# Kernel tuning notes

Measured on AMD Instinct MI355X. Metric: run time of the kernel, lower is better.

The kernel has to match this reference:

```python
import jax, jax.numpy as jnp
import numpy as np

N, DEG, F_IN, H = 50000, 16, 128, 32
E = N * DEG


def _linear_params(key, out_f, in_f):
    kw, kb = jax.random.split(key)
    s = 1.0 / np.sqrt(in_f)
    W = jax.random.uniform(kw, (out_f, in_f), jnp.float32, -s, s)
    b = jax.random.uniform(kb, (out_f,), jnp.float32, -s, s)
    return W, b


def setup_inputs() -> dict:
    key = jax.random.key(0)
    ks = jax.random.split(key, 12)
    X = jax.random.normal(ks[0], (N, F_IN), jnp.float32)
    # DEG distinct nonzero offsets shared by all rows -> unique (src,dst) pairs,
    # so the COO tensor is already coalesced (no duplicate indices).
    offsets = jax.random.permutation(ks[1], jnp.arange(1, N))[:DEG]
    src = jnp.repeat(jnp.arange(N, dtype=jnp.int32), DEG)
    dst = ((src.reshape(N, DEG) + offsets[None, :].astype(jnp.int32)) % N).reshape(-1)
    D = jax.ops.segment_sum(jnp.ones((E,), jnp.float32), src, num_segments=N)
    wn1p, bn1p = _linear_params(ks[2], H, F_IN)      # convN1.pass_map
    wn1s, bn1s = _linear_params(ks[3], H, F_IN)      # convN1.self_map
    we1p, be1p = _linear_params(ks[4], H, 2 * H)     # convE1.pass_map
    we1s, be1s = _linear_params(ks[5], H, F_IN)      # convE1.self_map
    wn2p, bn2p = _linear_params(ks[6], H, H)         # convN2.pass_map
    wn2s, bn2s = _linear_params(ks[7], H, H)         # convN2.self_map
    we2p, be2p = _linear_params(ks[8], H, 2 * H)     # convE2.pass_map
    we2s, be2s = _linear_params(ks[9], H, H)         # convE2.self_map
    wc, bc = _linear_params(ks[10], 1, H)            # classifier
    return dict(X=X, src=src, dst=dst, D=D,
                wn1p=wn1p, bn1p=bn1p, wn1s=wn1s, bn1s=bn1s,
                we1p=we1p, be1p=be1p, we1s=we1s, be1s=be1s,
                wn2p=wn2p, bn2p=bn2p, wn2s=wn2s, bn2s=bn2s,
                we2p=we2p, be2p=be2p, we2s=we2s, be2s=be2s,
                wc=wc, bc=bc)


def reference(X, src, dst, D,
              wn1p, bn1p, wn1s, bn1s,
              we1p, be1p, we1s, be1s,
              wn2p, bn2p, wn2s, bn2s,
              we2p, be2p, we2s, be2s,
              wc, bc):
    n = X.shape[0]

    def node_conv(vals, Xn, wp, bp, ws, bs):
        # torch.sparse.sum(A, dim=1): sum edge values per source row
        Asum = jax.ops.segment_sum(vals, src, num_segments=n)
        return jax.nn.relu((Asum / D[:, None]) @ wp.T + bp + Xn @ ws.T + bs)

    def edge_conv(vals, Xn, wp, bp, ws, bs):
        X1, X2 = Xn[src], Xn[dst]
        Ef = jnp.concatenate([(X1 - X2) * 0.5, (X1 + X2) * 0.5], axis=-1)
        return jax.nn.relu(Ef @ wp.T + bp + vals @ ws.T + bs)

    # add_graph: edge features = |X[src] - X[dst]|
    vals0 = jnp.abs(X[src] - X[dst])            # (E, F_IN)
    X0 = jnp.zeros_like(X)                       # forward zeros node features
    Xn1 = node_conv(vals0, X0, wn1p, bn1p, wn1s, bn1s)   # (N, 32)
    vals1 = edge_conv(vals0, Xn1, we1p, be1p, we1s, be1s)  # (E, 32)
    Xn2 = node_conv(vals1, Xn1, wn2p, bn2p, wn2s, bn2s)  # (N, 32)
    vals2 = edge_conv(vals1, Xn2, we2p, be2p, we2s, be2s)  # (E, 32)
    SX = jax.nn.sigmoid(vals2 @ wc.T + bc)[:, 0]          # (E,)
    return SX
```

## Files before the change

kernel.cpp:

```cpp
#include <hip/hip_runtime.h>

#define DEG 16
#define F_IN 128
#define H 32
#define CH 16

typedef __attribute__((ext_vector_type(8))) _Float16 f16x8;
typedef __attribute__((ext_vector_type(4))) float f32x4;
typedef __attribute__((ext_vector_type(4))) int i32x4;

union HF4 { _Float16 h[4]; uint2 u; };
union HS  { _Float16 f; unsigned short s; };

__device__ __forceinline__ float relu_f(float x) { return fmaxf(x, 0.0f); }

__device__ __forceinline__ f16x8 habs8(f16x8 a) {
    union { f16x8 h; i32x4 i; } u; u.h = a;
#pragma unroll
    for (int k = 0; k < 4; ++k) u.i[k] &= 0x7FFF7FFF;
    return u.h;
}
__device__ __forceinline__ unsigned short f2h_s(float x) {
    HS v; v.f = (_Float16)x; return v.s;
}
__device__ __forceinline__ float h2f_s(unsigned short s) {
    HS v; v.s = s; return (float)v.f;
}

__global__ __launch_bounds__(256) void k_xhalf(
    const float* __restrict__ X, _Float16* __restrict__ Xh, long n8)
{
    const long t = (long)blockIdx.x * 256 + threadIdx.x;
    if (t >= n8) return;
    const float4* p = (const float4*)X + t * 2;
    const float4 a = p[0], b = p[1];
    f16x8 h;
    h[0] = (_Float16)a.x; h[1] = (_Float16)a.y; h[2] = (_Float16)a.z; h[3] = (_Float16)a.w;
    h[4] = (_Float16)b.x; h[5] = (_Float16)b.y; h[6] = (_Float16)b.z; h[7] = (_Float16)b.w;
    *(f16x8*)(Xh + t * 8) = h;
}

__global__ __launch_bounds__(256) void k_prep(
    const float* __restrict__ we1s, const float* __restrict__ we1p,
    const float* __restrict__ be1p, const float* __restrict__ be1s,
    const float* __restrict__ we2p, const float* __restrict__ we2s,
    const float* __restrict__ be2p, const float* __restrict__ be2s,
    const float* __restrict__ wn1p, const float* __restrict__ bn1p,
    const float* __restrict__ bn1s,
    const float* __restrict__ wn2p, const float* __restrict__ bn2p,
    const float* __restrict__ wn2s, const float* __restrict__ bn2s,
    _Float16* __restrict__ Wcat1, _Float16* __restrict__ Wcat2,
    _Float16* __restrict__ Wn1ph,
    _Float16* __restrict__ Wn2ph, _Float16* __restrict__ Wn2sh,
    float* __restrict__ bias1, float* __restrict__ bias2,
    float* __restrict__ biasn1, float* __restrict__ biasn2)
{
    const int tid = threadIdx.x;
    for (int idx = tid; idx < 32 * 192; idx += 256) {
        const int n = idx / 192, k = idx - n * 192;
        float w;
        if (k < 128)       w = we1s[n * 128 + k];
        else if (k < 160)  w = 0.5f * we1p[n * 64 + (k - 128)];
        else               w = 0.5f * we1p[n * 64 + 32 + (k - 160)];
        Wcat1[idx] = (_Float16)w;
    }
    for (int idx = tid; idx < 32 * 96; idx += 256) {
        const int n = idx / 96, k = idx - n * 96;
        float w;
        if (k < 32)       w = 0.5f * we2p[n * 64 + k];
        else if (k < 64)  w = 0.5f * we2p[n * 64 + 32 + (k - 32)];
        else              w = we2s[n * 32 + (k - 64)];
        Wcat2[idx] = (_Float16)w;
    }
    for (int idx = tid; idx < 32 * 128; idx += 256)
        Wn1ph[idx] = (_Float16)wn1p[idx];
    for (int idx = tid; idx < 32 * 32; idx += 256) {
        Wn2ph[idx] = (_Float16)wn2p[idx];
        Wn2sh[idx] = (_Float16)wn2s[idx];
    }
    if (tid < H) {
        bias1[tid]  = be1p[tid] + be1s[tid];
        bias2[tid]  = be2p[tid] + be2s[tid];
        biasn1[tid] = bn1p[tid] + bn1s[tid];
        biasn2[tid] = bn2p[tid] + bn2s[tid];
    }
}

__global__ __launch_bounds__(256) void k_p1(
    const _Float16* __restrict__ Xh, const int* __restrict__ dst,
    const float* __restrict__ D,
    const _Float16* __restrict__ Wcat1, const _Float16* __restrict__ Wn1ph,
    const float* __restrict__ biasn1,
    _Float16* __restrict__ t1h, _Float16* __restrict__ Xn1h, int N)
{
    __shared__ int dsL[16 * 17];
    __shared__ float UacS[4][16 * 33];
    const int tid = threadIdx.x;
    const int wave = tid >> 6, lane = tid & 63;
    const int i0 = blockIdx.x * CH;
    {
        const int mm = tid >> 4, j = tid & 15;
        const int nd = (i0 + mm < N) ? (i0 + mm) : (N - 1);
        dsL[mm * 17 + j] = dst[nd * DEG + j];
    }
    __syncthreads();
    const int m = lane & 15, g = lane >> 4;
    const int srow = (i0 + m < N) ? (i0 + m) : (N - 1);

    f16x8 sv[4];
#pragma unroll
    for (int kb = 0; kb < 4; ++kb)
        sv[kb] = *(const f16x8*)(Xh + (size_t)srow * F_IN + kb * 32 + g * 8);
    int dj[4];
#pragma unroll
    for (int jj = 0; jj < 4; ++jj) dj[jj] = dsL[m * 17 + wave * 4 + jj];
    f16x8 tv[4][4];
#pragma unroll
    for (int jj = 0; jj < 4; ++jj)
#pragma unroll
        for (int kb = 0; kb < 4; ++kb)
            tv[jj][kb] = *(const f16x8*)(Xh + (size_t)dj[jj] * F_IN + kb * 32 + g * 8);
    f16x8 Bs[4][2], Bn[4][2];
#pragma unroll
    for (int kb = 0; kb < 4; ++kb)
#pragma unroll
        for (int t = 0; t < 2; ++t) {
            Bs[kb][t] = *(const f16x8*)(Wcat1 + (t * 16 + m) * 192 + kb * 32 + g * 8);
            Bn[kb][t] = *(const f16x8*)(Wn1ph + (t * 16 + m) * 128 + kb * 32 + g * 8);
        }

    f32x4 cn0 = {0.f,0.f,0.f,0.f}, cn1 = {0.f,0.f,0.f,0.f};
#pragma unroll
    for (int jj = 0; jj < 4; ++jj) {
        f32x4 cs0 = {0.f,0.f,0.f,0.f}, cs1 = {0.f,0.f,0.f,0.f};
#pragma unroll
        for (int kb = 0; kb < 4; ++kb) {
            const f16x8 a = habs8(sv[kb] - tv[jj][kb]);
            cs0 = __builtin_amdgcn_mfma_f32_16x16x32_f16(a, Bs[kb][0], cs0, 0, 0, 0);
            cs1 = __builtin_amdgcn_mfma_f32_16x16x32_f16(a, Bs[kb][1], cs1, 0, 0, 0);
            cn0 = __builtin_amdgcn_mfma_f32_16x16x32_f16(a, Bn[kb][0], cn0, 0, 0, 0);
            cn1 = __builtin_amdgcn_mfma_f32_16x16x32_f16(a, Bn[kb][1], cn1, 0, 0, 0);
        }
        const size_t tb = ((size_t)blockIdx.x * 16 + wave * 4 + jj) * 512;
        HF4 a;
#pragma unroll
        for (int r = 0; r < 4; ++r) a.h[r] = (_Float16)cs0[r];
        *(uint2*)(t1h + tb + lane * 4) = a.u;
#pragma unroll
        for (int r = 0; r < 4; ++r) a.h[r] = (_Float16)cs1[r];
        *(uint2*)(t1h + tb + 256 + lane * 4) = a.u;
    }
#pragma unroll
    for (int r = 0; r < 4; ++r) {
        UacS[wave][(g * 4 + r) * 33 + m]      = cn0[r];
        UacS[wave][(g * 4 + r) * 33 + 16 + m] = cn1[r];
    }
    __syncthreads();
    {
        const int mm = tid >> 4, c = tid & 15;
        float u0 = 0.f, u1 = 0.f;
#pragma unroll
        for (int w = 0; w < 4; ++w) {
            u0 += UacS[w][mm * 33 + c];
            u1 += UacS[w][mm * 33 + 16 + c];
        }
        if (i0 + mm < N) {
            const float invD = 1.0f / D[i0 + mm];
            Xn1h[(size_t)(i0 + mm) * H + c]      = (_Float16)relu_f(u0 * invD + biasn1[c]);
            Xn1h[(size_t)(i0 + mm) * H + 16 + c] = (_Float16)relu_f(u1 * invD + biasn1[16 + c]);
        }
    }
}

__global__ __launch_bounds__(256) void k_p2(
    const int* __restrict__ dst, const _Float16* __restrict__ Xn1h,
    const _Float16* __restrict__ Wcat1, const float* __restrict__ bias1,
    const _Float16* __restrict__ Wn2ph, const _Float16* __restrict__ Wn2sh,
    const float* __restrict__ biasn2, const float* __restrict__ D,
    _Float16* t1v1,
    _Float16* __restrict__ Xn2h, int N)
{
    __shared__ int dsL[16 * 17];
    __shared__ unsigned short RP[4][16 * 40];
    __shared__ float AacS[4][16 * 33];
    __shared__ unsigned short AsumH[16 * 40];
    const int tid = threadIdx.x;
    const int wave = tid >> 6, lane = tid & 63;
    const int i0 = blockIdx.x * CH;
    {
        const int mm = tid >> 4, j = tid & 15;
        const int nd = (i0 + mm < N) ? (i0 + mm) : (N - 1);
        dsL[mm * 17 + j] = dst[nd * DEG + j];
    }
    __syncthreads();
    const int m = lane & 15, g = lane >> 4;
    const int srow = (i0 + m < N) ? (i0 + m) : (N - 1);

    const f16x8 x1 = *(const f16x8*)(Xn1h + (size_t)srow * H + g * 8);
    int dj[4];
#pragma unroll
    for (int jj = 0; jj < 4; ++jj) dj[jj] = dsL[m * 17 + wave * 4 + jj];
    f16x8 x2[4];
#pragma unroll
    for (int jj = 0; jj < 4; ++jj)
        x2[jj] = *(const f16x8*)(Xn1h + (size_t)dj[jj] * H + g * 8);
    uint2 ta[4], tbv[4];
#pragma unroll
    for (int jj = 0; jj < 4; ++jj) {
        const size_t tb = ((size_t)blockIdx.x * 16 + wave * 4 + jj) * 512;
        ta[jj]  = *(const uint2*)(t1v1 + tb + lane * 4);
        tbv[jj] = *(const uint2*)(t1v1 + tb + 256 + lane * 4);
    }
    f16x8 Bf[2][2];
#pragma unroll
    for (int kb = 0; kb < 2; ++kb)
#pragma unroll
        for (int t = 0; t < 2; ++t)
            Bf[kb][t] = *(const f16x8*)(Wcat1 + (t * 16 + m) * 192 + (4 + kb) * 32 + g * 8);

    const float b0 = bias1[m], b1v = bias1[16 + m];
    float sA0[4] = {0.f,0.f,0.f,0.f}, sA1[4] = {0.f,0.f,0.f,0.f};
    unsigned short* L = RP[wave];
#pragma unroll
    for (int jj = 0; jj < 4; ++jj) {
        f32x4 c0, c1;
        { HF4 a; a.u = ta[jj];
#pragma unroll
          for (int r = 0; r < 4; ++r) c0[r] = (float)a.h[r];
          a.u = tbv[jj];
#pragma unroll
          for (int r = 0; r < 4; ++r) c1[r] = (float)a.h[r]; }
        const f16x8 ad = x1 - x2[jj];
        const f16x8 aS = x1 + x2[jj];
        c0 = __builtin_amdgcn_mfma_f32_16x16x32_f16(ad, Bf[0][0], c0, 0, 0, 0);
        c1 = __builtin_amdgcn_mfma_f32_16x16x32_f16(ad, Bf[0][1], c1, 0, 0, 0);
        c0 = __builtin_amdgcn_mfma_f32_16x16x32_f16(aS, Bf[1][0], c0, 0, 0, 0);
        c1 = __builtin_amdgcn_mfma_f32_16x16x32_f16(aS, Bf[1][1], c1, 0, 0, 0);
#pragma unroll
        for (int r = 0; r < 4; ++r) {
            const float v0 = relu_f(c0[r] + b0);
            const float v1 = relu_f(c1[r] + b1v);
            L[(g * 4 + r) * 40 + m]      = f2h_s(v0);
            L[(g * 4 + r) * 40 + 16 + m] = f2h_s(v1);
            sA0[r] += v0; sA1[r] += v1;
        }
        const size_t tb = ((size_t)blockIdx.x * 16 + wave * 4 + jj) * 512;
        const int rr = lane >> 2, q = lane & 3;
        const i32x4 v = *(const i32x4*)(L + rr * 40 + q * 8);
        *(i32x4*)(t1v1 + tb + rr * 32 + q * 8) = v;
    }
#pragma unroll
    for (int r = 0; r < 4; ++r) {
        AacS[wave][(g * 4 + r) * 33 + m]      = sA0[r];
        AacS[wave][(g * 4 + r) * 33 + 16 + m] = sA1[r];
    }
    __syncthreads();
    {
        const int mm = tid >> 4, c = tid & 15;
        float a0 = 0.f, a1 = 0.f;
#pragma unroll
        for (int w = 0; w < 4; ++w) {
            a0 += AacS[w][mm * 33 + c];
            a1 += AacS[w][mm * 33 + 16 + c];
        }
        const int nd = (i0 + mm < N) ? (i0 + mm) : (N - 1);
        const float invD = 1.0f / D[nd];
        AsumH[mm * 40 + c]      = f2h_s(a0 * invD);
        AsumH[mm * 40 + 16 + c] = f2h_s(a1 * invD);
    }
    __syncthreads();
    if (wave == 0) {
        const f16x8 aF = *(const f16x8*)((const _Float16*)AsumH + m * 40 + g * 8);
        f16x8 Bp[2], Bs2[2];
#pragma unroll
        for (int t = 0; t < 2; ++t) {
            Bp[t]  = *(const f16x8*)(Wn2ph + (t * 16 + m) * H + g * 8);
            Bs2[t] = *(const f16x8*)(Wn2sh + (t * 16 + m) * H + g * 8);
        }
        f32x4 c0 = {0.f,0.f,0.f,0.f}, c1 = {0.f,0.f,0.f,0.f};
        c0 = __builtin_amdgcn_mfma_f32_16x16x32_f16(aF, Bp[0], c0, 0, 0, 0);
        c1 = __builtin_amdgcn_mfma_f32_16x16x32_f16(aF, Bp[1], c1, 0, 0, 0);
        c0 = __builtin_amdgcn_mfma_f32_16x16x32_f16(x1, Bs2[0], c0, 0, 0, 0);
        c1 = __builtin_amdgcn_mfma_f32_16x16x32_f16(x1, Bs2[1], c1, 0, 0, 0);
        const float bp0 = biasn2[m], bp1 = biasn2[16 + m];
#pragma unroll
        for (int r = 0; r < 4; ++r) {
            const int node = i0 + g * 4 + r;
            if (node < N) {
                Xn2h[(size_t)node * H + m]      = (_Float16)relu_f(c0[r] + bp0);
                Xn2h[(size_t)node * H + 16 + m] = (_Float16)relu_f(c1[r] + bp1);
            }
        }
    }
}

__global__ __launch_bounds__(256) void k_p3(
    const _Float16* __restrict__ Xn2h, const int* __restrict__ dst,
    const _Float16* __restrict__ vals1,
    const _Float16* __restrict__ Wcat2, const float* __restrict__ bias2,
    const float* __restrict__ wc, const float* __restrict__ bc,
    float* __restrict__ out, int N)
{
    __shared__ int dsL[16 * 17];
    __shared__ float outS[16 * 17];
    const int tid = threadIdx.x;
    const int wave = tid >> 6, lane = tid & 63;
    const int i0 = blockIdx.x * CH;
    {
        const int mm = tid >> 4, j = tid & 15;
        const int nd = (i0 + mm < N) ? (i0 + mm) : (N - 1);
        dsL[mm * 17 + j] = dst[nd * DEG + j];
    }
    __syncthreads();
    const int m = lane & 15, g = lane >> 4;
    const int srow = (i0 + m < N) ? (i0 + m) : (N - 1);

    const f16x8 x1 = *(const f16x8*)(Xn2h + (size_t)srow * H + g * 8);
    int dj[4];
#pragma unroll
    for (int jj = 0; jj < 4; ++jj) dj[jj] = dsL[m * 17 + wave * 4 + jj];
    f16x8 x2[4], av[4];
#pragma unroll
    for (int jj = 0; jj < 4; ++jj) {
        x2[jj] = *(const f16x8*)(Xn2h + (size_t)dj[jj] * H + g * 8);
        const size_t tb = ((size_t)blockIdx.x * 16 + wave * 4 + jj) * 512;
        av[jj] = *(const f16x8*)(vals1 + tb + m * 32 + g * 8);
    }
    f16x8 Bf[3][2];
#pragma unroll
    for (int kb = 0; kb < 3; ++kb)
#pragma unroll
        for (int t = 0; t < 2; ++t)
            Bf[kb][t] = *(const f16x8*)(Wcat2 + (t * 16 + m) * 96 + kb * 32 + g * 8);

    const float b0 = bias2[m], b1v = bias2[16 + m];
    const float w0 = wc[m], w1 = wc[16 + m];
#pragma unroll
    for (int jj = 0; jj < 4; ++jj) {
        const f16x8 ad = x1 - x2[jj];
        const f16x8 aS = x1 + x2[jj];
        f32x4 c0 = {0.f,0.f,0.f,0.f}, c1 = {0.f,0.f,0.f,0.f};
        c0 = __builtin_amdgcn_mfma_f32_16x16x32_f16(ad,     Bf[0][0], c0, 0, 0, 0);
        c1 = __builtin_amdgcn_mfma_f32_16x16x32_f16(ad,     Bf[0][1], c1, 0, 0, 0);
        c0 = __builtin_amdgcn_mfma_f32_16x16x32_f16(aS,     Bf[1][0], c0, 0, 0, 0);
        c1 = __builtin_amdgcn_mfma_f32_16x16x32_f16(aS,     Bf[1][1], c1, 0, 0, 0);
        c0 = __builtin_amdgcn_mfma_f32_16x16x32_f16(av[jj], Bf[2][0], c0, 0, 0, 0);
        c1 = __builtin_amdgcn_mfma_f32_16x16x32_f16(av[jj], Bf[2][1], c1, 0, 0, 0);

        float sr[4];
#pragma unroll
        for (int r = 0; r < 4; ++r)
            sr[r] = relu_f(c0[r] + b0) * w0 + relu_f(c1[r] + b1v) * w1;
#pragma unroll
        for (int mask = 1; mask < 16; mask <<= 1) {
#pragma unroll
            for (int r = 0; r < 4; ++r)
                sr[r] += __shfl_xor(sr[r], mask);
        }
        if (m == 0) {
#pragma unroll
            for (int r = 0; r < 4; ++r)
                outS[(g * 4 + r) * 17 + (wave * 4 + jj)] = sr[r];
        }
    }
    __syncthreads();
    {
        const int mm = tid >> 4;
        if (i0 + mm < N) {
            const float sx = outS[mm * 17 + (tid & 15)] + bc[0];
            out[(size_t)i0 * DEG + tid] = 1.0f / (1.0f + __expf(-sx));
        }
    }
}

extern "C" void kernel_launch(void* const* d_in, const int* in_sizes, int n_in,
                              void* d_out, int out_size, void* d_ws, size_t ws_size,
                              hipStream_t stream)
{
    const float* X    = (const float*)d_in[0];
    const int*   dst  = (const int*)  d_in[2];
    const float* D    = (const float*)d_in[3];
    const float* wn1p = (const float*)d_in[4];
    const float* bn1p = (const float*)d_in[5];
    const float* bn1s = (const float*)d_in[7];
    const float* we1p = (const float*)d_in[8];
    const float* be1p = (const float*)d_in[9];
    const float* we1s = (const float*)d_in[10];
    const float* be1s = (const float*)d_in[11];
    const float* wn2p = (const float*)d_in[12];
    const float* bn2p = (const float*)d_in[13];
    const float* wn2s = (const float*)d_in[14];
    const float* bn2s = (const float*)d_in[15];
    const float* we2p = (const float*)d_in[16];
    const float* be2p = (const float*)d_in[17];
    const float* we2s = (const float*)d_in[18];
    const float* be2s = (const float*)d_in[19];
    const float* wc   = (const float*)d_in[20];
    const float* bc   = (const float*)d_in[21];

    const int N = in_sizes[3];
    const int nbC = (N + CH - 1) / CH;
    const size_t Epad = (size_t)nbC * CH * DEG;

    char* w = (char*)d_ws;
    _Float16* t1v1  = (_Float16*)w;  w += Epad * H * 2;
    _Float16* Xh    = (_Float16*)w;  w += (size_t)N * F_IN * 2;
    _Float16* Xn1h  = (_Float16*)w;  w += (size_t)N * H * 2;
    _Float16* Xn2h  = (_Float16*)w;  w += (size_t)N * H * 2;
    _Float16* Wcat1 = (_Float16*)w;  w += 32 * 192 * 2;
    _Float16* Wcat2 = (_Float16*)w;  w += 32 * 96 * 2;
    _Float16* Wn1ph = (_Float16*)w;  w += 32 * 128 * 2;
    _Float16* Wn2ph = (_Float16*)w;  w += 32 * 32 * 2;
    _Float16* Wn2sh = (_Float16*)w;  w += 32 * 32 * 2;
    float* bias1  = (float*)w;       w += H * 4;
    float* bias2  = (float*)w;       w += H * 4;
    float* biasn1 = (float*)w;       w += H * 4;
    float* biasn2 = (float*)w;       w += H * 4;
    float* outp = (float*)d_out;

    const long n8 = (long)N * F_IN / 8;
    const int nbX = (int)((n8 + 255) / 256);

    k_xhalf<<<nbX, 256, 0, stream>>>(X, Xh, n8);
    k_prep<<<1, 256, 0, stream>>>(we1s, we1p, be1p, be1s, we2p, we2s, be2p, be2s,
                                  wn1p, bn1p, bn1s, wn2p, bn2p, wn2s, bn2s,
                                  Wcat1, Wcat2, Wn1ph, Wn2ph, Wn2sh,
                                  bias1, bias2, biasn1, biasn2);
    k_p1<<<nbC, 256, 0, stream>>>(Xh, dst, D, Wcat1, Wn1ph, biasn1, t1v1, Xn1h, N);
    k_p2<<<nbC, 256, 0, stream>>>(dst, Xn1h, Wcat1, bias1, Wn2ph, Wn2sh, biasn2, D,
                                  t1v1, Xn2h, N);
    k_p3<<<nbC, 256, 0, stream>>>(Xn2h, dst, t1v1, Wcat2, bias2, wc, bc, outp, N);
}
```

Baseline: 227.5 us.

## Recompute edge self-map in p2 instead of storing intermediate, prefetch gathers

The first edge-conv self-map product (|X[src]-X[dst]| @ we1s^T) is no longer computed in k_p1 and written to a global buffer, then read back in k_p2. k_p2 now regathers the fp16 X rows and recomputes it with MFMA, trading an E×32 fp16 write plus read for a second 128-wide gather of X. Both kernels also software-prefetch the next neighbor's X row while the current one is processed. The shared-memory dst staging and its barrier are replaced by direct per-lane loads, and the weight-prep kernel is spread over 32 blocks.

```diff
diff --git a/kernel.cpp b/kernel.cpp
--- a/kernel.cpp
+++ b/kernel.cpp
@@ -9,8 +9,7 @@
 typedef __attribute__((ext_vector_type(4))) float f32x4;
 typedef __attribute__((ext_vector_type(4))) int i32x4;
 
-union HF4 { _Float16 h[4]; uint2 u; };
-union HS  { _Float16 f; unsigned short s; };
+union HS { _Float16 f; unsigned short s; };
 
 __device__ __forceinline__ float relu_f(float x) { return fmaxf(x, 0.0f); }
 
@@ -22,9 +21,6 @@
 }
 __device__ __forceinline__ unsigned short f2h_s(float x) {
     HS v; v.f = (_Float16)x; return v.s;
-}
-__device__ __forceinline__ float h2f_s(unsigned short s) {
-    HS v; v.s = s; return (float)v.f;
 }
 
 __global__ __launch_bounds__(256) void k_xhalf(
@@ -55,8 +51,9 @@
     float* __restrict__ bias1, float* __restrict__ bias2,
     float* __restrict__ biasn1, float* __restrict__ biasn2)
 {
-    const int tid = threadIdx.x;
-    for (int idx = tid; idx < 32 * 192; idx += 256) {
+    const int t0 = blockIdx.x * 256 + threadIdx.x;
+    const int stride = gridDim.x * 256;
+    for (int idx = t0; idx < 32 * 192; idx += stride) {
         const int n = idx / 192, k = idx - n * 192;
         float w;
         if (k < 128)       w = we1s[n * 128 + k];
@@ -64,7 +61,7 @@
         else               w = 0.5f * we1p[n * 64 + 32 + (k - 160)];
         Wcat1[idx] = (_Float16)w;
     }
-    for (int idx = tid; idx < 32 * 96; idx += 256) {
+    for (int idx = t0; idx < 32 * 96; idx += stride) {
         const int n = idx / 96, k = idx - n * 96;
         float w;
         if (k < 32)       w = 0.5f * we2p[n * 64 + k];
@@ -72,83 +69,70 @@
         else              w = we2s[n * 32 + (k - 64)];
         Wcat2[idx] = (_Float16)w;
     }
-    for (int idx = tid; idx < 32 * 128; idx += 256)
+    for (int idx = t0; idx < 32 * 128; idx += stride)
         Wn1ph[idx] = (_Float16)wn1p[idx];
-    for (int idx = tid; idx < 32 * 32; idx += 256) {
+    for (int idx = t0; idx < 32 * 32; idx += stride) {
         Wn2ph[idx] = (_Float16)wn2p[idx];
         Wn2sh[idx] = (_Float16)wn2s[idx];
     }
-    if (tid < H) {
-        bias1[tid]  = be1p[tid] + be1s[tid];
-        bias2[tid]  = be2p[tid] + be2s[tid];
-        biasn1[tid] = bn1p[tid] + bn1s[tid];
-        biasn2[tid] = bn2p[tid] + bn2s[tid];
+    if (t0 < H) {
+        bias1[t0]  = be1p[t0] + be1s[t0];
+        bias2[t0]  = be2p[t0] + be2s[t0];
+        biasn1[t0] = bn1p[t0] + bn1s[t0];
+        biasn2[t0] = bn2p[t0] + bn2s[t0];
     }
 }
 
 __global__ __launch_bounds__(256) void k_p1(
     const _Float16* __restrict__ Xh, const int* __restrict__ dst,
     const float* __restrict__ D,
-    const _Float16* __restrict__ Wcat1, const _Float16* __restrict__ Wn1ph,
-    const float* __restrict__ biasn1,
-    _Float16* __restrict__ t1h, _Float16* __restrict__ Xn1h, int N)
-{
-    __shared__ int dsL[16 * 17];
+    const _Float16* __restrict__ Wn1ph, const float* __restrict__ biasn1,
+    _Float16* __restrict__ Xn1h, int N)
+{
     __shared__ float UacS[4][16 * 33];
     const int tid = threadIdx.x;
     const int wave = tid >> 6, lane = tid & 63;
     const int i0 = blockIdx.x * CH;
-    {
-        const int mm = tid >> 4, j = tid & 15;
-        const int nd = (i0 + mm < N) ? (i0 + mm) : (N - 1);
-        dsL[mm * 17 + j] = dst[nd * DEG + j];
-    }
-    __syncthreads();
     const int m = lane & 15, g = lane >> 4;
     const int srow = (i0 + m < N) ? (i0 + m) : (N - 1);
 
+    int dj[4];
+#pragma unroll
+    for (int jj = 0; jj < 4; ++jj)
+        dj[jj] = dst[(size_t)srow * DEG + wave * 4 + jj];
+
     f16x8 sv[4];
 #pragma unroll
     for (int kb = 0; kb < 4; ++kb)
         sv[kb] = *(const f16x8*)(Xh + (size_t)srow * F_IN + kb * 32 + g * 8);
-    int dj[4];
-#pragma unroll
-    for (int jj = 0; jj < 4; ++jj) dj[jj] = dsL[m * 17 + wave * 4 + jj];
-    f16x8 tv[4][4];
-#pragma unroll
-    for (int jj = 0; jj < 4; ++jj)
-#pragma unroll
-        for (int kb = 0; kb < 4; ++kb)
-            tv[jj][kb] = *(const f16x8*)(Xh + (size_t)dj[jj] * F_IN + kb * 32 + g * 8);
-    f16x8 Bs[4][2], Bn[4][2];
+    f16x8 Bn[4][2];
 #pragma unroll
     for (int kb = 0; kb < 4; ++kb)
 #pragma unroll
-        for (int t = 0; t < 2; ++t) {
-            Bs[kb][t] = *(const f16x8*)(Wcat1 + (t * 16 + m) * 192 + kb * 32 + g * 8);
+        for (int t = 0; t < 2; ++t)
             Bn[kb][t] = *(const f16x8*)(Wn1ph + (t * 16 + m) * 128 + kb * 32 + g * 8);
-        }
+
+    f16x8 tvc[4], tvn[4];
+#pragma unroll
+    for (int kb = 0; kb < 4; ++kb)
+        tvc[kb] = *(const f16x8*)(Xh + (size_t)dj[0] * F_IN + kb * 32 + g * 8);
 
     f32x4 cn0 = {0.f,0.f,0.f,0.f}, cn1 = {0.f,0.f,0.f,0.f};
 #pragma unroll
     for (int jj = 0; jj < 4; ++jj) {
-        f32x4 cs0 = {0.f,0.f,0.f,0.f}, cs1 = {0.f,0.f,0.f,0.f};
+        if (jj < 3) {
+#pragma unroll
+            for (int kb = 0; kb < 4; ++kb)
+                tvn[kb] = *(const f16x8*)(Xh + (size_t)dj[jj + 1] * F_IN + kb * 32 + g * 8);
+        }
 #pragma unroll
         for (int kb = 0; kb < 4; ++kb) {
-            const f16x8 a = habs8(sv[kb] - tv[jj][kb]);
-            cs0 = __builtin_amdgcn_mfma_f32_16x16x32_f16(a, Bs[kb][0], cs0, 0, 0, 0);
-            cs1 = __builtin_amdgcn_mfma_f32_16x16x32_f16(a, Bs[kb][1], cs1, 0, 0, 0);
+            const f16x8 a = habs8(sv[kb] - tvc[kb]);
             cn0 = __builtin_amdgcn_mfma_f32_16x16x32_f16(a, Bn[kb][0], cn0, 0, 0, 0);
             cn1 = __builtin_amdgcn_mfma_f32_16x16x32_f16(a, Bn[kb][1], cn1, 0, 0, 0);
         }
-        const size_t tb = ((size_t)blockIdx.x * 16 + wave * 4 + jj) * 512;
-        HF4 a;
-#pragma unroll
-        for (int r = 0; r < 4; ++r) a.h[r] = (_Float16)cs0[r];
-        *(uint2*)(t1h + tb + lane * 4) = a.u;
-#pragma unroll
-        for (int r = 0; r < 4; ++r) a.h[r] = (_Float16)cs1[r];
-        *(uint2*)(t1h + tb + 256 + lane * 4) = a.u;
+#pragma unroll
+        for (int kb = 0; kb < 4; ++kb) tvc[kb] = tvn[kb];
     }
 #pragma unroll
     for (int r = 0; r < 4; ++r) {
@@ -173,69 +157,71 @@
 }
 
 __global__ __launch_bounds__(256) void k_p2(
-    const int* __restrict__ dst, const _Float16* __restrict__ Xn1h,
+    const _Float16* __restrict__ Xh, const int* __restrict__ dst,
+    const _Float16* __restrict__ Xn1h,
     const _Float16* __restrict__ Wcat1, const float* __restrict__ bias1,
     const _Float16* __restrict__ Wn2ph, const _Float16* __restrict__ Wn2sh,
     const float* __restrict__ biasn2, const float* __restrict__ D,
-    _Float16* t1v1,
-    _Float16* __restrict__ Xn2h, int N)
-{
-    __shared__ int dsL[16 * 17];
+    _Float16* __restrict__ vals1, _Float16* __restrict__ Xn2h, int N)
+{
     __shared__ unsigned short RP[4][16 * 40];
     __shared__ float AacS[4][16 * 33];
     __shared__ unsigned short AsumH[16 * 40];
     const int tid = threadIdx.x;
     const int wave = tid >> 6, lane = tid & 63;
     const int i0 = blockIdx.x * CH;
-    {
-        const int mm = tid >> 4, j = tid & 15;
-        const int nd = (i0 + mm < N) ? (i0 + mm) : (N - 1);
-        dsL[mm * 17 + j] = dst[nd * DEG + j];
-    }
-    __syncthreads();
     const int m = lane & 15, g = lane >> 4;
     const int srow = (i0 + m < N) ? (i0 + m) : (N - 1);
 
+    int dj[4];
+#pragma unroll
+    for (int jj = 0; jj < 4; ++jj)
+        dj[jj] = dst[(size_t)srow * DEG + wave * 4 + jj];
+
     const f16x8 x1 = *(const f16x8*)(Xn1h + (size_t)srow * H + g * 8);
-    int dj[4];
-#pragma unroll
-    for (int jj = 0; jj < 4; ++jj) dj[jj] = dsL[m * 17 + wave * 4 + jj];
     f16x8 x2[4];
 #pragma unroll
     for (int jj = 0; jj < 4; ++jj)
         x2[jj] = *(const f16x8*)(Xn1h + (size_t)dj[jj] * H + g * 8);
-    uint2 ta[4], tbv[4];
-#pragma unroll
-    for (int jj = 0; jj < 4; ++jj) {
-        const size_t tb = ((size_t)blockIdx.x * 16 + wave * 4 + jj) * 512;
-        ta[jj]  = *(const uint2*)(t1v1 + tb + lane * 4);
-        tbv[jj] = *(const uint2*)(t1v1 + tb + 256 + lane * 4);
-    }
-    f16x8 Bf[2][2];
-#pragma unroll
-    for (int kb = 0; kb < 2; ++kb)
+    f16x8 sv[4];
+#pragma unroll
+    for (int kb = 0; kb < 4; ++kb)
+        sv[kb] = *(const f16x8*)(Xh + (size_t)srow * F_IN + kb * 32 + g * 8);
+    f16x8 Bf[6][2];
+#pragma unroll
+    for (int kb = 0; kb < 6; ++kb)
 #pragma unroll
         for (int t = 0; t < 2; ++t)
-            Bf[kb][t] = *(const f16x8*)(Wcat1 + (t * 16 + m) * 192 + (4 + kb) * 32 + g * 8);
+            Bf[kb][t] = *(const f16x8*)(Wcat1 + (t * 16 + m) * 192 + kb * 32 + g * 8);
+
+    f16x8 tvc[4], tvn[4];
+#pragma unroll
+    for (int kb = 0; kb < 4; ++kb)
+        tvc[kb] = *(const f16x8*)(Xh + (size_t)dj[0] * F_IN + kb * 32 + g * 8);
 
     const float b0 = bias1[m], b1v = bias1[16 + m];
     float sA0[4] = {0.f,0.f,0.f,0.f}, sA1[4] = {0.f,0.f,0.f,0.f};
     unsigned short* L = RP[wave];
 #pragma unroll
     for (int jj = 0; jj < 4; ++jj) {
-        f32x4 c0, c1;
-        { HF4 a; a.u = ta[jj];
-#pragma unroll
-          for (int r = 0; r < 4; ++r) c0[r] = (float)a.h[r];
-          a.u = tbv[jj];
-#pragma unroll
-          for (int r = 0; r < 4; ++r) c1[r] = (float)a.h[r]; }
+        if (jj < 3) {
+#pragma unroll
+            for (int kb = 0; kb < 4; ++kb)
+                tvn[kb] = *(const f16x8*)(Xh + (size_t)dj[jj + 1] * F_IN + kb * 32 + g * 8);
+        }
+        f32x4 c0 = {0.f,0.f,0.f,0.f}, c1 = {0.f,0.f,0.f,0.f};
+#pragma unroll
+        for (int kb = 0; kb < 4; ++kb) {
+            const f16x8 a = habs8(sv[kb] - tvc[kb]);
+            c0 = __builtin_amdgcn_mfma_f32_16x16x32_f16(a, Bf[kb][0], c0, 0, 0, 0);
+            c1 = __builtin_amdgcn_mfma_f32_16x16x32_f16(a, Bf[kb][1], c1, 0, 0, 0);
+        }
         const f16x8 ad = x1 - x2[jj];
         const f16x8 aS = x1 + x2[jj];
-        c0 = __builtin_amdgcn_mfma_f32_16x16x32_f16(ad, Bf[0][0], c0, 0, 0, 0);
-        c1 = __builtin_amdgcn_mfma_f32_16x16x32_f16(ad, Bf[0][1], c1, 0, 0, 0);
-        c0 = __builtin_amdgcn_mfma_f32_16x16x32_f16(aS, Bf[1][0], c0, 0, 0, 0);
-        c1 = __builtin_amdgcn_mfma_f32_16x16x32_f16(aS, Bf[1][1], c1, 0, 0, 0);
+        c0 = __builtin_amdgcn_mfma_f32_16x16x32_f16(ad, Bf[4][0], c0, 0, 0, 0);
+        c1 = __builtin_amdgcn_mfma_f32_16x16x32_f16(ad, Bf[4][1], c1, 0, 0, 0);
+        c0 = __builtin_amdgcn_mfma_f32_16x16x32_f16(aS, Bf[5][0], c0, 0, 0, 0);
+        c1 = __builtin_amdgcn_mfma_f32_16x16x32_f16(aS, Bf[5][1], c1, 0, 0, 0);
 #pragma unroll
         for (int r = 0; r < 4; ++r) {
             const float v0 = relu_f(c0[r] + b0);
@@ -247,7 +233,9 @@
         const size_t tb = ((size_t)blockIdx.x * 16 + wave * 4 + jj) * 512;
         const int rr = lane >> 2, q = lane & 3;
         const i32x4 v = *(const i32x4*)(L + rr * 40 + q * 8);
-        *(i32x4*)(t1v1 + tb + rr * 32 + q * 8) = v;
+        *(i32x4*)(vals1 + tb + rr * 32 + q * 8) = v;
+#pragma unroll
+        for (int kb = 0; kb < 4; ++kb) tvc[kb] = tvn[kb];
     }
 #pragma unroll
     for (int r = 0; r < 4; ++r) {
@@ -301,24 +289,19 @@
     const float* __restrict__ wc, const float* __restrict__ bc,
     float* __restrict__ out, int N)
 {
-    __shared__ int dsL[16 * 17];
     __shared__ float outS[16 * 17];
     const int tid = threadIdx.x;
     const int wave = tid >> 6, lane = tid & 63;
     const int i0 = blockIdx.x * CH;
-    {
-        const int mm = tid >> 4, j = tid & 15;
-        const int nd = (i0 + mm < N) ? (i0 + mm) : (N - 1);
-        dsL[mm * 17 + j] = dst[nd * DEG + j];
-    }
-    __syncthreads();
     const int m = lane & 15, g = lane >> 4;
     const int srow = (i0 + m < N) ? (i0 + m) : (N - 1);
 
+    int dj[4];
+#pragma unroll
+    for (int jj = 0; jj < 4; ++jj)
+        dj[jj] = dst[(size_t)srow * DEG + wave * 4 + jj];
+
     const f16x8 x1 = *(const f16x8*)(Xn2h + (size_t)srow * H + g * 8);
-    int dj[4];
-#pragma unroll
-    for (int jj = 0; jj < 4; ++jj) dj[jj] = dsL[m * 17 + wave * 4 + jj];
     f16x8 x2[4], av[4];
 #pragma unroll
     for (int jj = 0; jj < 4; ++jj) {
@@ -403,7 +386,7 @@
     const size_t Epad = (size_t)nbC * CH * DEG;
 
     char* w = (char*)d_ws;
-    _Float16* t1v1  = (_Float16*)w;  w += Epad * H * 2;
+    _Float16* vals1 = (_Float16*)w;  w += Epad * H * 2;
     _Float16* Xh    = (_Float16*)w;  w += (size_t)N * F_IN * 2;
     _Float16* Xn1h  = (_Float16*)w;  w += (size_t)N * H * 2;
     _Float16* Xn2h  = (_Float16*)w;  w += (size_t)N * H * 2;
@@ -422,12 +405,12 @@
     const int nbX = (int)((n8 + 255) / 256);
 
     k_xhalf<<<nbX, 256, 0, stream>>>(X, Xh, n8);
-    k_prep<<<1, 256, 0, stream>>>(we1s, we1p, be1p, be1s, we2p, we2s, be2p, be2s,
-                                  wn1p, bn1p, bn1s, wn2p, bn2p, wn2s, bn2s,
-                                  Wcat1, Wcat2, Wn1ph, Wn2ph, Wn2sh,
-                                  bias1, bias2, biasn1, biasn2);
-    k_p1<<<nbC, 256, 0, stream>>>(Xh, dst, D, Wcat1, Wn1ph, biasn1, t1v1, Xn1h, N);
-    k_p2<<<nbC, 256, 0, stream>>>(dst, Xn1h, Wcat1, bias1, Wn2ph, Wn2sh, biasn2, D,
-                                  t1v1, Xn2h, N);
-    k_p3<<<nbC, 256, 0, stream>>>(Xn2h, dst, t1v1, Wcat2, bias2, wc, bc, outp, N);
-}
+    k_prep<<<32, 256, 0, stream>>>(we1s, we1p, be1p, be1s, we2p, we2s, be2p, be2s,
+                                   wn1p, bn1p, bn1s, wn2p, bn2p, wn2s, bn2s,
+                                   Wcat1, Wcat2, Wn1ph, Wn2ph, Wn2sh,
+                                   bias1, bias2, biasn1, biasn2);
+    k_p1<<<nbC, 256, 0, stream>>>(Xh, dst, D, Wn1ph, biasn1, Xn1h, N);
+    k_p2<<<nbC, 256, 0, stream>>>(Xh, dst, Xn1h, Wcat1, bias1, Wn2ph, Wn2sh,
+                                  biasn2, D, vals1, Xn2h, N);
+    k_p3<<<nbC, 256, 0, stream>>>(Xn2h, dst, vals1, Wcat2, bias2, wc, bc, outp, N);
+}
```

Result: slower. 232.4 us (+2.2%).
